# Kernel tuning notes

Hardware: AMD Instinct MI355X
Metric: run time of the kernel (lower is better)

Reference implementation:

```python
import jax, jax.numpy as jnp
import numpy as np

B, H, Wd, C = 8, 64, 64, 128
KH, KW = 3, 3
N = KH * KW  # kernel_n
F = 256


def _grid_offset(h, w, kh, kw):
    """Replicates the TensorLayer grid construction exactly, including the
    (2,kh,kw)->(kh*kw,2) reshape of the stacked meshgrid."""
    n = kh * kw
    initial = np.stack(np.meshgrid(np.arange(kh), np.arange(kw), indexing='ij'))  # (2,kh,kw)
    initial = initial.reshape(-1, 2).astype(np.float32)  # (n,2), faithful flattening order
    gy = np.arange(-int((kh - 1) / 2.0), h - int((kh - 1) / 2.0))
    gx = np.arange(-int((kw - 1) / 2.0), w - int((kw - 1) / 2.0))
    grid = np.stack(np.meshgrid(gy, gx, indexing='ij'), axis=-1).astype(np.float32)  # (h,w,2)
    grid = np.tile(grid[:, :, None, :], (1, 1, n, 1))  # (h,w,n,2)
    return jnp.asarray(grid + initial[None, None, :, :])  # (h,w,n,2)


def setup_inputs() -> dict:
    key = jax.random.key(0)
    k1, k2, k3 = jax.random.split(key, 3)
    x = jax.random.normal(k1, (B, H, Wd, C), dtype=jnp.float32)
    offsets = jax.random.normal(k2, (B, H, Wd, 2 * N), dtype=jnp.float32)
    W = jax.random.normal(k3, (N, C, F), dtype=jnp.float32) * 0.02  # truncated_normal(0.02) analogue
    b = jnp.zeros((F,), dtype=jnp.float32)
    return {"x": x, "offsets": offsets, "W": W, "b": b}


def reference(x, offsets, W, b):
    h, w = x.shape[1], x.shape[2]
    grid = _grid_offset(h, w, KH, KW)  # (h,w,n,2)
    coords = grid[None] + offsets.reshape(x.shape[0], h, w, N, 2)  # (b,h,w,n,2)
    cy = jnp.clip(coords[..., 0], 0.0, jnp.float32(h - 1))
    cx = jnp.clip(coords[..., 1], 0.0, jnp.float32(w - 1))
    y0 = jnp.floor(cy).astype(jnp.int32)
    y1 = jnp.ceil(cy).astype(jnp.int32)
    x0 = jnp.floor(cx).astype(jnp.int32)
    x1 = jnp.ceil(cx).astype(jnp.int32)

    bidx = jnp.arange(x.shape[0])[:, None, None, None]

    def gather(yy, xx):
        return x[bidx, yy, xx]  # (b,h,w,n,c)

    v_lt = gather(y0, x0)
    v_rb = gather(y1, x1)
    v_lb = gather(y0, x1)  # (lt_y, rb_x) as in original
    v_rt = gather(y1, x0)  # (rb_y, lt_x) as in original

    fy = (cy - y0.astype(cy.dtype))[..., None]
    fx = (cx - x0.astype(cx.dtype))[..., None]
    vals_t = v_lt + (v_rt - v_lt) * fy
    vals_b = v_lb + (v_rb - v_lb) * fy
    mapped = vals_t + (vals_b - vals_t) * fx  # (b,h,w,n,c)

    # conv3d with kernel [1,1,n,c,f] + VALID == contraction over (n,c)
    out = jnp.einsum('bhwnc,ncf->bhwf', mapped, W) + b
    return out
```

## Files before the change

### kernel.cpp

```cpp
#include <hip/hip_runtime.h>

#define HH 64
#define WW 64
#define CC 128
#define FF 256
#define NTAP 9
#define KD 1152
#define XELEMS (8 * HH * WW * CC)
#define XCVT_BLOCKS (XELEMS / (256 * 8))
#define WT_BLOCKS 144

typedef __attribute__((ext_vector_type(8))) short bf16x8;
typedef __attribute__((ext_vector_type(4))) float floatx4;

__device__ inline unsigned short f2bf(float v) {
  union { float f; unsigned u; } c; c.f = v;
  unsigned r = (c.u + 0x7FFFu + ((c.u >> 16) & 1u)) >> 16;
  return (unsigned short)r;
}
__device__ inline float bflo(unsigned u) {
  union { unsigned u; float f; } c; c.u = u << 16; return c.f;
}
__device__ inline float bfhi(unsigned u) {
  union { unsigned u; float f; } c; c.u = u & 0xFFFF0000u; return c.f;
}
__device__ inline unsigned cvt_pk_bf16(float lo, float hi) {
  unsigned r;
  asm("v_cvt_pk_bf16_f32 %0, %1, %2" : "=v"(r) : "v"(lo), "v"(hi));
  return r;
}

__device__ inline unsigned lerp_word(unsigned u00, unsigned u10, unsigned u01, unsigned u11,
                                     float w00, float w10, float w01, float w11) {
  float rlo = bflo(u00) * w00 + bflo(u10) * w10 + bflo(u01) * w01 + bflo(u11) * w11;
  float rhi = bfhi(u00) * w00 + bfhi(u10) * w10 + bfhi(u01) * w01 + bfhi(u11) * w11;
  return cvt_pk_bf16(rlo, rhi);
}

#define IY_PACK 0x18690
#define IX_PACK 0x21894

struct ITap { int b00, b10, b01, b11; float fy, fx; };

__device__ inline ITap tap_from(float2 o2, int yy, int xx, int n) {
  float cy = (float)(yy - 1 + ((IY_PACK >> (2 * n)) & 3)) + o2.x;
  float cx = (float)(xx - 1 + ((IX_PACK >> (2 * n)) & 3)) + o2.y;
  cy = fminf(fmaxf(cy, 0.f), 63.f);
  cx = fminf(fmaxf(cx, 0.f), 63.f);
  const float fy0 = floorf(cy), fx0 = floorf(cx);
  const int y0 = (int)fy0, y1 = (int)ceilf(cy);
  const int x0 = (int)fx0, x1 = (int)ceilf(cx);
  ITap t;
  t.b00 = (y0 * WW + x0) * CC;
  t.b10 = (y1 * WW + x0) * CC;
  t.b01 = (y0 * WW + x1) * CC;
  t.b11 = (y1 * WW + x1) * CC;
  t.fy = cy - fy0;
  t.fx = cx - fx0;
  return t;
}

__global__ void prep_kernel(const float* __restrict__ X, const float* __restrict__ W,
                            unsigned short* __restrict__ Xb, unsigned short* __restrict__ Wtf) {
  const int blk = blockIdx.x;
  if (blk < XCVT_BLOCKS) {
    const int t = blk * 256 + threadIdx.x;
    const float4* src = (const float4*)(X + (size_t)t * 8);
    float4 a = src[0], b2 = src[1];
    bf16x8 o;
    o[0] = (short)f2bf(a.x);  o[1] = (short)f2bf(a.y);
    o[2] = (short)f2bf(a.z);  o[3] = (short)f2bf(a.w);
    o[4] = (short)f2bf(b2.x); o[5] = (short)f2bf(b2.y);
    o[6] = (short)f2bf(b2.z); o[7] = (short)f2bf(b2.w);
    *(bf16x8*)(Xb + (size_t)t * 8) = o;
  } else {
    const int t = (blk - XCVT_BLOCKS) * 256 + threadIdx.x;
    const int f  = t & 255;
    const int kc = t >> 8;
    unsigned short o[8];
#pragma unroll
    for (int j = 0; j < 8; ++j)
      o[j] = f2bf(W[(size_t)(kc * 8 + j) * FF + f]);
    const int kt = kc >> 3, ks = (kc >> 2) & 1, aq = kc & 3;
    const int fg = f >> 6, ft = (f >> 4) & 3, arow = f & 15;
    const size_t addr = (size_t)((kt * 2 + ks) * 16 + fg * 4 + ft) * 512 + aq * 128 + arow * 8;
    *(uint4*)(Wtf + addr) = *(uint4*)o;
  }
}

__global__ __launch_bounds__(256, 4) void fused_kernel(
    const unsigned short* __restrict__ Xb, const float* __restrict__ Off,
    const unsigned short* __restrict__ Wtf, const float* __restrict__ bias,
    float* __restrict__ Out)
{
  __shared__ unsigned short smA[2][32 * 64];

  const int blk = blockIdx.x;
  const int b   = blk & 7;
  const int i   = blk >> 3;
  const int y   = i >> 1;
  const int m0  = b * 4096 + i * 32;
  const int tid = threadIdx.x;
  const int wave = tid >> 6, lane = tid & 63;
  const int arow = lane & 15, aq = lane >> 4;
  const int p   = tid >> 3;
  const int c0  = tid & 7;
  const int px  = (i & 1) * 32 + p;

  const unsigned short* xb   = Xb + (size_t)b * (HH * WW * CC);
  const float* offp          = Off + ((size_t)(b * HH + y) * WW + px) * (2 * NTAP);
  const unsigned short* wbase = Wtf + (size_t)wave * 2048 + (size_t)lane * 8;

  floatx4 acc[2][4];
#pragma unroll
  for (int mt = 0; mt < 2; ++mt)
#pragma unroll
    for (int ft = 0; ft < 4; ++ft)
      acc[mt][ft] = (floatx4){0.f, 0.f, 0.f, 0.f};

  const int sa_off = p * 64 + ((c0 ^ (p & 7)) << 3);

  ITap tL = tap_from(*(const float2*)offp, y, px, 0);
  uint4 g0, g1, g2, g3;
  {
    const int ch = c0 * 8;
    uint4 q00 = *(const uint4*)(xb + tL.b00 + ch);
    uint4 q10 = *(const uint4*)(xb + tL.b10 + ch);
    uint4 q01 = *(const uint4*)(xb + tL.b01 + ch);
    uint4 q11 = *(const uint4*)(xb + tL.b11 + ch);
    const float gy = 1.f - tL.fy, gx = 1.f - tL.fx;
    const float w00 = gy * gx, w10 = tL.fy * gx, w01 = gy * tL.fx, w11 = tL.fy * tL.fx;
    uint4 o;
    o.x = lerp_word(q00.x, q10.x, q01.x, q11.x, w00, w10, w01, w11);
    o.y = lerp_word(q00.y, q10.y, q01.y, q11.y, w00, w10, w01, w11);
    o.z = lerp_word(q00.z, q10.z, q01.z, q11.z, w00, w10, w01, w11);
    o.w = lerp_word(q00.w, q10.w, q01.w, q11.w, w00, w10, w01, w11);
    *(uint4*)&smA[0][sa_off] = o;
    const int ch1 = (8 + c0) * 8;
    g0 = *(const uint4*)(xb + tL.b00 + ch1);
    g1 = *(const uint4*)(xb + tL.b10 + ch1);
    g2 = *(const uint4*)(xb + tL.b01 + ch1);
    g3 = *(const uint4*)(xb + tL.b11 + ch1);
  }
  ITap tG = tL;
  __syncthreads();

  int cur = 0;
  for (int kt = 0; kt < 18; ++kt) {
    const unsigned short* wk = wbase + (size_t)kt * 16384;

    bf16x8 b0[4], b1[4];
#pragma unroll
    for (int ft = 0; ft < 4; ++ft)
      b0[ft] = *(const bf16x8*)(wk + ft * 512);

    bf16x8 afr[2][2];
#pragma unroll
    for (int ks = 0; ks < 2; ++ks) {
      const int slot = (((ks * 4 + aq) ^ (arow & 7)) << 3);
#pragma unroll
      for (int mt = 0; mt < 2; ++mt)
        afr[ks][mt] = *(const bf16x8*)&smA[cur][(mt * 16 + arow) * 64 + slot];
    }

    if (kt <= 16) {
      const float gy = 1.f - tL.fy, gx = 1.f - tL.fx;
      const float w00 = gy * gx, w10 = tL.fy * gx, w01 = gy * tL.fx, w11 = tL.fy * tL.fx;
      uint4 o;
      o.x = lerp_word(g0.x, g1.x, g2.x, g3.x, w00, w10, w01, w11);
      o.y = lerp_word(g0.y, g1.y, g2.y, g3.y, w00, w10, w01, w11);
      o.z = lerp_word(g0.z, g1.z, g2.z, g3.z, w00, w10, w01, w11);
      o.w = lerp_word(g0.w, g1.w, g2.w, g3.w, w00, w10, w01, w11);
      *(uint4*)&smA[cur ^ 1][sa_off] = o;
    }

#pragma unroll
    for (int ft = 0; ft < 4; ++ft)
      b1[ft] = *(const bf16x8*)(wk + 8192 + ft * 512);

    if (kt <= 15) {
      if ((kt & 1) == 0)
        tG = tap_from(*(const float2*)(offp + 2 * ((kt + 2) >> 1)), y, px, (kt + 2) >> 1);
      const int ch = ((kt & 1) * 8 + c0) * 8;
      g0 = *(const uint4*)(xb + tG.b00 + ch);
      g1 = *(const uint4*)(xb + tG.b10 + ch);
      g2 = *(const uint4*)(xb + tG.b01 + ch);
      g3 = *(const uint4*)(xb + tG.b11 + ch);
    }

#pragma unroll
    for (int mt = 0; mt < 2; ++mt)
#pragma unroll
      for (int ft = 0; ft < 4; ++ft)
        acc[mt][ft] = __builtin_amdgcn_mfma_f32_16x16x32_bf16(
            afr[0][mt], b0[ft], acc[mt][ft], 0, 0, 0);
#pragma unroll
    for (int mt = 0; mt < 2; ++mt)
#pragma unroll
      for (int ft = 0; ft < 4; ++ft)
        acc[mt][ft] = __builtin_amdgcn_mfma_f32_16x16x32_bf16(
            afr[1][mt], b1[ft], acc[mt][ft], 0, 0, 0);

    __syncthreads();
    cur ^= 1;
    tL = tG;
  }

  float bv[4];
#pragma unroll
  for (int ft = 0; ft < 4; ++ft)
    bv[ft] = bias[wave * 64 + ft * 16 + arow];
#pragma unroll
  for (int mt = 0; mt < 2; ++mt) {
#pragma unroll
    for (int ft = 0; ft < 4; ++ft) {
      const int f = wave * 64 + ft * 16 + arow;
#pragma unroll
      for (int r = 0; r < 4; ++r) {
        const int m = m0 + mt * 16 + aq * 4 + r;
        Out[(size_t)m * FF + f] = acc[mt][ft][r] + bv[ft];
      }
    }
  }
}

extern "C" void kernel_launch(void* const* d_in, const int* in_sizes, int n_in,
                              void* d_out, int out_size, void* d_ws, size_t ws_size,
                              hipStream_t stream) {
  const float* X    = (const float*)d_in[0];
  const float* Off  = (const float*)d_in[1];
  const float* W    = (const float*)d_in[2];
  const float* bias = (const float*)d_in[3];
  float* Out = (float*)d_out;

  unsigned short* Wtf = (unsigned short*)d_ws;
  unsigned short* Xb  = Wtf + (size_t)FF * KD;

  prep_kernel<<<XCVT_BLOCKS + WT_BLOCKS, 256, 0, stream>>>(X, W, Xb, Wtf);
  fused_kernel<<<1024, 256, 0, stream>>>(Xb, Off, Wtf, bias, Out);
}
```

Baseline: 110.1 us.

## Double M-tile per block to 64 pixels, reusing weight fragments across more rows

```diff
diff --git a/kernel.cpp b/kernel.cpp
--- a/kernel.cpp
+++ b/kernel.cpp
@@ -88,59 +88,64 @@
   }
 }
 
-__global__ __launch_bounds__(256, 4) void fused_kernel(
+__global__ __launch_bounds__(256, 2) void fused_kernel(
     const unsigned short* __restrict__ Xb, const float* __restrict__ Off,
     const unsigned short* __restrict__ Wtf, const float* __restrict__ bias,
     float* __restrict__ Out)
 {
-  __shared__ unsigned short smA[2][32 * 64];
+  __shared__ unsigned short smA[2][64 * 64];
 
   const int blk = blockIdx.x;
   const int b   = blk & 7;
-  const int i   = blk >> 3;
-  const int y   = i >> 1;
-  const int m0  = b * 4096 + i * 32;
+  const int y   = blk >> 3;
+  const int m0  = b * 4096 + y * 64;
   const int tid = threadIdx.x;
   const int wave = tid >> 6, lane = tid & 63;
   const int arow = lane & 15, aq = lane >> 4;
-  const int p   = tid >> 3;
-  const int c0  = tid & 7;
-  const int px  = (i & 1) * 32 + p;
-
-  const unsigned short* xb   = Xb + (size_t)b * (HH * WW * CC);
-  const float* offp          = Off + ((size_t)(b * HH + y) * WW + px) * (2 * NTAP);
+  const int p   = tid >> 2;
+  const int c0  = tid & 3;
+
+  const unsigned short* xb    = Xb + (size_t)b * (HH * WW * CC);
+  const float* offp           = Off + ((size_t)(b * HH + y) * WW + p) * (2 * NTAP);
   const unsigned short* wbase = Wtf + (size_t)wave * 2048 + (size_t)lane * 8;
 
-  floatx4 acc[2][4];
-#pragma unroll
-  for (int mt = 0; mt < 2; ++mt)
+  floatx4 acc[4][4];
+#pragma unroll
+  for (int mt = 0; mt < 4; ++mt)
 #pragma unroll
     for (int ft = 0; ft < 4; ++ft)
       acc[mt][ft] = (floatx4){0.f, 0.f, 0.f, 0.f};
 
-  const int sa_off = p * 64 + ((c0 ^ (p & 7)) << 3);
-
-  ITap tL = tap_from(*(const float2*)offp, y, px, 0);
-  uint4 g0, g1, g2, g3;
+  const int sa0 = p * 64 + ((c0 ^ (p & 7)) << 3);
+  const int sa1 = p * 64 + (((c0 + 4) ^ (p & 7)) << 3);
+
+  ITap tL = tap_from(*(const float2*)offp, y, p, 0);
+  uint4 g[2][4];
   {
-    const int ch = c0 * 8;
-    uint4 q00 = *(const uint4*)(xb + tL.b00 + ch);
-    uint4 q10 = *(const uint4*)(xb + tL.b10 + ch);
-    uint4 q01 = *(const uint4*)(xb + tL.b01 + ch);
-    uint4 q11 = *(const uint4*)(xb + tL.b11 + ch);
     const float gy = 1.f - tL.fy, gx = 1.f - tL.fx;
     const float w00 = gy * gx, w10 = tL.fy * gx, w01 = gy * tL.fx, w11 = tL.fy * tL.fx;
-    uint4 o;
-    o.x = lerp_word(q00.x, q10.x, q01.x, q11.x, w00, w10, w01, w11);
-    o.y = lerp_word(q00.y, q10.y, q01.y, q11.y, w00, w10, w01, w11);
-    o.z = lerp_word(q00.z, q10.z, q01.z, q11.z, w00, w10, w01, w11);
-    o.w = lerp_word(q00.w, q10.w, q01.w, q11.w, w00, w10, w01, w11);
-    *(uint4*)&smA[0][sa_off] = o;
-    const int ch1 = (8 + c0) * 8;
-    g0 = *(const uint4*)(xb + tL.b00 + ch1);
-    g1 = *(const uint4*)(xb + tL.b10 + ch1);
-    g2 = *(const uint4*)(xb + tL.b01 + ch1);
-    g3 = *(const uint4*)(xb + tL.b11 + ch1);
+#pragma unroll
+    for (int cc = 0; cc < 2; ++cc) {
+      const int ch = (c0 + cc * 4) * 8;
+      uint4 q00 = *(const uint4*)(xb + tL.b00 + ch);
+      uint4 q10 = *(const uint4*)(xb + tL.b10 + ch);
+      uint4 q01 = *(const uint4*)(xb + tL.b01 + ch);
+      uint4 q11 = *(const uint4*)(xb + tL.b11 + ch);
+      uint4 o;
+      o.x = lerp_word(q00.x, q10.x, q01.x, q11.x, w00, w10, w01, w11);
+      o.y = lerp_word(q00.y, q10.y, q01.y, q11.y, w00, w10, w01, w11);
+      o.z = lerp_word(q00.z, q10.z, q01.z, q11.z, w00, w10, w01, w11);
+      o.w = lerp_word(q00.w, q10.w, q01.w, q11.w, w00, w10, w01, w11);
+      *(uint4*)&smA[0][cc ? sa1 : sa0] = o;
+    }
+#pragma unroll
+    for (int cc = 0; cc < 2; ++cc) {
+      const int ch1 = (8 + c0 + cc * 4) * 8;
+      g[cc][0] = *(const uint4*)(xb + tL.b00 + ch1);
+      g[cc][1] = *(const uint4*)(xb + tL.b10 + ch1);
+      g[cc][2] = *(const uint4*)(xb + tL.b01 + ch1);
+      g[cc][3] = *(const uint4*)(xb + tL.b11 + ch1);
+    }
   }
   ITap tG = tL;
   __syncthreads();
@@ -154,53 +159,67 @@
     for (int ft = 0; ft < 4; ++ft)
       b0[ft] = *(const bf16x8*)(wk + ft * 512);
 
-    bf16x8 afr[2][2];
+    bf16x8 afr[2][4];
 #pragma unroll
     for (int ks = 0; ks < 2; ++ks) {
       const int slot = (((ks * 4 + aq) ^ (arow & 7)) << 3);
 #pragma unroll
-      for (int mt = 0; mt < 2; ++mt)
+      for (int mt = 0; mt < 4; ++mt)
         afr[ks][mt] = *(const bf16x8*)&smA[cur][(mt * 16 + arow) * 64 + slot];
+    }
+
+#pragma unroll
+    for (int ft = 0; ft < 4; ++ft)
+      b1[ft] = *(const bf16x8*)(wk + 8192 + ft * 512);
+
+    uint4 gn[2][4];
+    if (kt <= 15) {
+      if ((kt & 1) == 0)
+        tG = tap_from(*(const float2*)(offp + 2 * ((kt + 2) >> 1)), y, p, (kt + 2) >> 1);
+#pragma unroll
+      for (int cc = 0; cc < 2; ++cc) {
+        const int ch = ((kt & 1) * 8 + c0 + cc * 4) * 8;
+        gn[cc][0] = *(const uint4*)(xb + tG.b00 + ch);
+        gn[cc][1] = *(const uint4*)(xb + tG.b10 + ch);
+        gn[cc][2] = *(const uint4*)(xb + tG.b01 + ch);
+        gn[cc][3] = *(const uint4*)(xb + tG.b11 + ch);
+      }
     }
 
     if (kt <= 16) {
       const float gy = 1.f - tL.fy, gx = 1.f - tL.fx;
       const float w00 = gy * gx, w10 = tL.fy * gx, w01 = gy * tL.fx, w11 = tL.fy * tL.fx;
-      uint4 o;
-      o.x = lerp_word(g0.x, g1.x, g2.x, g3.x, w00, w10, w01, w11);
-      o.y = lerp_word(g0.y, g1.y, g2.y, g3.y, w00, w10, w01, w11);
-      o.z = lerp_word(g0.z, g1.z, g2.z, g3.z, w00, w10, w01, w11);
-      o.w = lerp_word(g0.w, g1.w, g2.w, g3.w, w00, w10, w01, w11);
-      *(uint4*)&smA[cur ^ 1][sa_off] = o;
-    }
-
-#pragma unroll
-    for (int ft = 0; ft < 4; ++ft)
-      b1[ft] = *(const bf16x8*)(wk + 8192 + ft * 512);
-
-    if (kt <= 15) {
-      if ((kt & 1) == 0)
-        tG = tap_from(*(const float2*)(offp + 2 * ((kt + 2) >> 1)), y, px, (kt + 2) >> 1);
-      const int ch = ((kt & 1) * 8 + c0) * 8;
-      g0 = *(const uint4*)(xb + tG.b00 + ch);
-      g1 = *(const uint4*)(xb + tG.b10 + ch);
-      g2 = *(const uint4*)(xb + tG.b01 + ch);
-      g3 = *(const uint4*)(xb + tG.b11 + ch);
-    }
-
-#pragma unroll
-    for (int mt = 0; mt < 2; ++mt)
+#pragma unroll
+      for (int cc = 0; cc < 2; ++cc) {
+        uint4 o;
+        o.x = lerp_word(g[cc][0].x, g[cc][1].x, g[cc][2].x, g[cc][3].x, w00, w10, w01, w11);
+        o.y = lerp_word(g[cc][0].y, g[cc][1].y, g[cc][2].y, g[cc][3].y, w00, w10, w01, w11);
+        o.z = lerp_word(g[cc][0].z, g[cc][1].z, g[cc][2].z, g[cc][3].z, w00, w10, w01, w11);
+        o.w = lerp_word(g[cc][0].w, g[cc][1].w, g[cc][2].w, g[cc][3].w, w00, w10, w01, w11);
+        *(uint4*)&smA[cur ^ 1][cc ? sa1 : sa0] = o;
+      }
+    }
+
+#pragma unroll
+    for (int mt = 0; mt < 4; ++mt)
 #pragma unroll
       for (int ft = 0; ft < 4; ++ft)
         acc[mt][ft] = __builtin_amdgcn_mfma_f32_16x16x32_bf16(
             afr[0][mt], b0[ft], acc[mt][ft], 0, 0, 0);
 #pragma unroll
-    for (int mt = 0; mt < 2; ++mt)
+    for (int mt = 0; mt < 4; ++mt)
 #pragma unroll
       for (int ft = 0; ft < 4; ++ft)
         acc[mt][ft] = __builtin_amdgcn_mfma_f32_16x16x32_bf16(
             afr[1][mt], b1[ft], acc[mt][ft], 0, 0, 0);
 
+    if (kt <= 15) {
+#pragma unroll
+      for (int cc = 0; cc < 2; ++cc)
+#pragma unroll
+        for (int q2 = 0; q2 < 4; ++q2)
+          g[cc][q2] = gn[cc][q2];
+    }
     __syncthreads();
     cur ^= 1;
     tL = tG;
@@ -211,7 +230,7 @@
   for (int ft = 0; ft < 4; ++ft)
     bv[ft] = bias[wave * 64 + ft * 16 + arow];
 #pragma unroll
-  for (int mt = 0; mt < 2; ++mt) {
+  for (int mt = 0; mt < 4; ++mt) {
 #pragma unroll
     for (int ft = 0; ft < 4; ++ft) {
       const int f = wave * 64 + ft * 16 + arow;
@@ -237,5 +256,5 @@
   unsigned short* Xb  = Wtf + (size_t)FF * KD;
 
   prep_kernel<<<XCVT_BLOCKS + WT_BLOCKS, 256, 0, stream>>>(X, W, Xb, Wtf);
-  fused_kernel<<<1024, 256, 0, stream>>>(Xb, Off, Wtf, bias, Out);
-}
+  fused_kernel<<<512, 256, 0, stream>>>(Xb, Off, Wtf, bias, Out);
+}
```

After: 110.1 us. Within noise of the previous version (+0.0%).
